# Performance work log

Measured on AMD Instinct MI355X. Metric: run time of the kernel, lower is better.

## Reference

```python
import jax, jax.numpy as jnp
import numpy as np

NEG_SLOPE = 0.2
EPS = 1e-16


def _gat_conv(x_src, x_dst, src, dst, W_src, W_dst, a_src, a_dst, b):
    """Single-head bipartite GAT-style conv (gather-score-softmax-scatter)."""
    num_dst = x_dst.shape[0]
    h_src = x_src @ W_src                      # [Ns, C]
    h_dst = x_dst @ W_dst                      # [Nd, C]
    s_src = h_src @ a_src                      # [Ns]
    s_dst = h_dst @ a_dst                      # [Nd]
    e = jax.nn.leaky_relu(s_src[src] + s_dst[dst], NEG_SLOPE)  # [E]
    # segment softmax over incoming edges of each dst node
    m = jax.ops.segment_max(e, dst, num_segments=num_dst)      # [Nd]
    w = jnp.exp(e - m[dst])
    denom = jax.ops.segment_sum(w, dst, num_segments=num_dst)  # [Nd]
    alpha = w / (denom[dst] + EPS)                             # [E]
    out = jax.ops.segment_sum(alpha[:, None] * h_src[src], dst, num_segments=num_dst)
    return out + b


def setup_inputs() -> dict:
    key = jax.random.key(0)
    ks = jax.random.split(key, 32)
    N_a, N_p, N_v = 100000, 150000, 10000
    F_in, C = 768, 64
    E_w, E_c, E_p = 300000, 1500000, 150000
    sc_in = 1.0 / np.sqrt(F_in)
    sc_c = 1.0 / np.sqrt(C)
    inp = {
        'x_author': jax.random.normal(ks[0], (N_a, F_in), jnp.float32),
        'x_paper': jax.random.normal(ks[1], (N_p, F_in), jnp.float32),
        'x_venue': jax.random.normal(ks[2], (N_v, F_in), jnp.float32),
        'writes_src': jax.random.randint(ks[3], (E_w,), 0, N_a, jnp.int32),
        'writes_dst': jax.random.randint(ks[4], (E_w,), 0, N_p, jnp.int32),
        'cites_src': jax.random.randint(ks[5], (E_c,), 0, N_p, jnp.int32),
        'cites_dst': jax.random.randint(ks[6], (E_c,), 0, N_p, jnp.int32),
        'pub_src': jax.random.randint(ks[7], (E_p,), 0, N_v, jnp.int32),
        'pub_dst': jax.random.randint(ks[8], (E_p,), 0, N_p, jnp.int32),
    }
    # per-edge-type learned params: W_src, W_dst [F_in, C], att vecs [C], bias [C]
    names = ['w', 'c', 'p']  # writes, cites, publishes
    for i, n in enumerate(names):
        base = 9 + 5 * i
        inp[f'W{n}_src'] = jax.random.normal(ks[base + 0], (F_in, C), jnp.float32) * sc_in
        inp[f'W{n}_dst'] = jax.random.normal(ks[base + 1], (F_in, C), jnp.float32) * sc_in
        inp[f'a{n}_src'] = jax.random.normal(ks[base + 2], (C,), jnp.float32) * sc_c
        inp[f'a{n}_dst'] = jax.random.normal(ks[base + 3], (C,), jnp.float32) * sc_c
        inp[f'b{n}'] = jnp.zeros((C,), jnp.float32)
    return inp


def reference(x_author, x_paper, x_venue,
              writes_src, writes_dst, cites_src, cites_dst, pub_src, pub_dst,
              Ww_src, Ww_dst, aw_src, aw_dst, bw,
              Wc_src, Wc_dst, ac_src, ac_dst, bc,
              Wp_src, Wp_dst, ap_src, ap_dst, bp):
    # HeteroConv with aggr='sum': all three edge types target 'paper'
    out_w = _gat_conv(x_author, x_paper, writes_src, writes_dst, Ww_src, Ww_dst, aw_src, aw_dst, bw)
    out_c = _gat_conv(x_paper, x_paper, cites_src, cites_dst, Wc_src, Wc_dst, ac_src, ac_dst, bc)
    out_p = _gat_conv(x_venue, x_paper, pub_src, pub_dst, Wp_src, Wp_dst, ap_src, ap_dst, bp)
    return out_w + out_c + out_p  # [N_paper, out_channels]
```

## Files before the change

### kernel.cpp

```cpp
#include <hip/hip_runtime.h>


#define F_IN 768
#define C_OUT 64
#define BN 80
#define TILE_M 64
#define BK 64
#define LDK 72

typedef __bf16 bf16x8 __attribute__((ext_vector_type(8)));
typedef float  f32x4  __attribute__((ext_vector_type(4)));

__global__ void prep_weights(
    const float* __restrict__ Ww_src, const float* __restrict__ aw_src,
    const float* __restrict__ Wc_src, const float* __restrict__ ac_src,
    const float* __restrict__ Wp_src, const float* __restrict__ ap_src,
    const float* __restrict__ Ww_dst, const float* __restrict__ aw_dst,
    const float* __restrict__ Wc_dst, const float* __restrict__ ac_dst,
    const float* __restrict__ Wp_dst, const float* __restrict__ ap_dst,
    __bf16* __restrict__ WTw, __bf16* __restrict__ WTc, __bf16* __restrict__ WTp)
{
    int type = blockIdx.x;
    const float* Ws = (type == 0) ? Ww_src : (type == 1) ? Wc_src : Wp_src;
    const float* as = (type == 0) ? aw_src : (type == 1) ? ac_src : ap_src;
    __bf16* WT = (type == 0) ? WTw : (type == 1) ? WTc : WTp;

    for (int r = threadIdx.x; r < F_IN; r += blockDim.x) {
        const float* wrow = Ws + (size_t)r * C_OUT;
        float u = 0.f;
        for (int c = 0; c < C_OUT; ++c) {
            float wv = wrow[c];
            WT[(size_t)c * F_IN + r] = (__bf16)wv;
            u += wv * as[c];
        }
        WT[(size_t)64 * F_IN + r] = (__bf16)u;
        for (int c = 65; c < BN; ++c) WT[(size_t)c * F_IN + r] = (__bf16)0.f;
        if (type == 1) {
            const float* r1 = Ww_dst + (size_t)r * C_OUT;
            const float* r2 = Wc_dst + (size_t)r * C_OUT;
            const float* r3 = Wp_dst + (size_t)r * C_OUT;
            float vw = 0.f, vc = 0.f, vp = 0.f;
            for (int c = 0; c < C_OUT; ++c) {
                vw += r1[c] * aw_dst[c];
                vc += r2[c] * ac_dst[c];
                vp += r3[c] * ap_dst[c];
            }
            WT[(size_t)65 * F_IN + r] = (__bf16)vw;
            WT[(size_t)66 * F_IN + r] = (__bf16)vc;
            WT[(size_t)67 * F_IN + r] = (__bf16)vp;
        }
    }
}

__global__ __launch_bounds__(256) void gemm_fused(
    const float* __restrict__ X, const __bf16* __restrict__ WT,
    float* __restrict__ H,
    float* __restrict__ s0, float* __restrict__ s1,
    float* __restrict__ s2, float* __restrict__ s3, int M)
{
    __shared__ __bf16 As[TILE_M][LDK];
    __shared__ __bf16 Bs[BN][LDK];

    const int tid  = threadIdx.x;
    const int lane = tid & 63;
    const int warp = tid >> 6;
    const int colq = lane & 15;
    const int quad = lane >> 4;
    const int rowBase = blockIdx.x * TILE_M;

    f32x4 acc[5];
#pragma unroll
    for (int t = 0; t < 5; ++t) acc[t] = (f32x4){0.f, 0.f, 0.f, 0.f};

    const int arow  = tid >> 2;
    const int akoff = (tid & 3) * 16;
    const int grow  = rowBase + arow;
    const bool rowOK = grow < M;
    const float* xrow = X + (size_t)grow * F_IN;

    for (int kc = 0; kc < F_IN; kc += BK) {
        f32x4 av[4];
        if (rowOK) {
            const f32x4* xp = (const f32x4*)(xrow + kc + akoff);
            av[0] = xp[0]; av[1] = xp[1]; av[2] = xp[2]; av[3] = xp[3];
        } else {
#pragma unroll
            for (int i = 0; i < 4; ++i) av[i] = (f32x4){0.f, 0.f, 0.f, 0.f};
        }
        bf16x8 cv[2];
#pragma unroll
        for (int i = 0; i < 4; ++i)
#pragma unroll
            for (int j = 0; j < 4; ++j)
                cv[i >> 1][(i & 1) * 4 + j] = (__bf16)av[i][j];
        *(bf16x8*)&As[arow][akoff]     = cv[0];
        *(bf16x8*)&As[arow][akoff + 8] = cv[1];

        for (int c = tid; c < (BN * BK / 8); c += 256) {
            int br = c >> 3, bo = (c & 7) * 8;
            *(bf16x8*)&Bs[br][bo] =
                *(const bf16x8*)&WT[(size_t)br * F_IN + kc + bo];
        }
        __syncthreads();

#pragma unroll
        for (int kk = 0; kk < BK; kk += 32) {
            bf16x8 a = *(const bf16x8*)&As[warp * 16 + colq][kk + quad * 8];
#pragma unroll
            for (int t = 0; t < 5; ++t) {
                bf16x8 b = *(const bf16x8*)&Bs[t * 16 + colq][kk + quad * 8];
                acc[t] = __builtin_amdgcn_mfma_f32_16x16x32_bf16(a, b, acc[t], 0, 0, 0);
            }
        }
        __syncthreads();
    }

    const int orow0 = rowBase + warp * 16 + quad * 4;
#pragma unroll
    for (int r = 0; r < 4; ++r) {
        int row = orow0 + r;
        if (row < M) {
#pragma unroll
            for (int t = 0; t < 4; ++t)
                H[(size_t)row * C_OUT + t * 16 + colq] = acc[t][r];
            if (colq < 4) {
                float* sp = (colq == 0) ? s0 : (colq == 1) ? s1 : (colq == 2) ? s2 : s3;
                if (sp) sp[row] = acc[4][r];
            }
        }
    }
}

__global__ void init_out(const float* __restrict__ bw, const float* __restrict__ bc,
                         const float* __restrict__ bp, float* __restrict__ out, int n)
{
    int i = blockIdx.x * blockDim.x + threadIdx.x;
    if (i < n) {
        int c = i & 63;
        out[i] = bw[c] + bc[c] + bp[c];
    }
}

__global__ void edge_score(const float* __restrict__ sS, const float* __restrict__ sD,
                           const int* __restrict__ src, const int* __restrict__ dst,
                           float* __restrict__ wbuf, float* __restrict__ denom, int E)
{
    int i = blockIdx.x * blockDim.x + threadIdx.x;
    int stride = gridDim.x * blockDim.x;
    for (; i < E; i += stride) {
        float e = sS[src[i]] + sD[dst[i]];
        e = (e >= 0.f) ? e : 0.2f * e;
        float w = __expf(e);
        wbuf[i] = w;
        atomicAdd(&denom[dst[i]], w);
    }
}

__global__ void edge_scatter(const float* __restrict__ H, const float* __restrict__ wbuf,
                             const float* __restrict__ denom, const int* __restrict__ src,
                             const int* __restrict__ dst, float* __restrict__ out, int E)
{
    const int lane = threadIdx.x & 63;
    int wid = (blockIdx.x * blockDim.x + threadIdx.x) >> 6;
    const int nw = (gridDim.x * blockDim.x) >> 6;
    for (int e = wid; e < E; e += nw) {
        int s = src[e], d = dst[e];
        float alpha = wbuf[e] / (denom[d] + 1e-16f);
        float v = H[(size_t)s * C_OUT + lane] * alpha;
        atomicAdd(&out[(size_t)d * C_OUT + lane], v);
    }
}

extern "C" void kernel_launch(void* const* d_in, const int* in_sizes, int n_in,
                              void* d_out, int out_size, void* d_ws, size_t ws_size,
                              hipStream_t stream)
{
    const float* x_a = (const float*)d_in[0];
    const float* x_p = (const float*)d_in[1];
    const float* x_v = (const float*)d_in[2];
    const int* w_src = (const int*)d_in[3];
    const int* w_dst = (const int*)d_in[4];
    const int* c_src = (const int*)d_in[5];
    const int* c_dst = (const int*)d_in[6];
    const int* p_src = (const int*)d_in[7];
    const int* p_dst = (const int*)d_in[8];
    const float* Ww_src = (const float*)d_in[9];
    const float* Ww_dst = (const float*)d_in[10];
    const float* aw_src = (const float*)d_in[11];
    const float* aw_dst = (const float*)d_in[12];
    const float* bw     = (const float*)d_in[13];
    const float* Wc_src = (const float*)d_in[14];
    const float* Wc_dst = (const float*)d_in[15];
    const float* ac_src = (const float*)d_in[16];
    const float* ac_dst = (const float*)d_in[17];
    const float* bc     = (const float*)d_in[18];
    const float* Wp_src = (const float*)d_in[19];
    const float* Wp_dst = (const float*)d_in[20];
    const float* ap_src = (const float*)d_in[21];
    const float* ap_dst = (const float*)d_in[22];
    const float* bp     = (const float*)d_in[23];
    float* out = (float*)d_out;

    const int Na = in_sizes[0] / F_IN;
    const int Np = in_sizes[1] / F_IN;
    const int Nv = in_sizes[2] / F_IN;
    const int Ew = in_sizes[3];
    const int Ec = in_sizes[5];
    const int Ep = in_sizes[7];

    char* ws = (char*)d_ws;
    size_t off = 0;
    auto alloc = [&](size_t bytes) -> void* {
        off = (off + 255) & ~(size_t)255;
        void* p = ws + off;
        off += bytes;
        return p;
    };
    __bf16* WTw = (__bf16*)alloc((size_t)BN * F_IN * 2);
    __bf16* WTc = (__bf16*)alloc((size_t)BN * F_IN * 2);
    __bf16* WTp = (__bf16*)alloc((size_t)BN * F_IN * 2);
    float* Ha = (float*)alloc((size_t)Na * C_OUT * 4);
    float* Hp = (float*)alloc((size_t)Np * C_OUT * 4);
    float* Hv = (float*)alloc((size_t)Nv * C_OUT * 4);
    float* s_w_src = (float*)alloc((size_t)Na * 4);
    float* s_c_src = (float*)alloc((size_t)Np * 4);
    float* s_p_src = (float*)alloc((size_t)Nv * 4);
    float* s_w_dst = (float*)alloc((size_t)Np * 4);
    float* s_c_dst = (float*)alloc((size_t)Np * 4);
    float* s_p_dst = (float*)alloc((size_t)Np * 4);
    float* den = (float*)alloc((size_t)3 * Np * 4);
    float* den_w = den, *den_c = den + Np, *den_p = den + 2 * Np;
    float* wb_w = (float*)alloc((size_t)Ew * 4);
    float* wb_c = (float*)alloc((size_t)Ec * 4);
    float* wb_p = (float*)alloc((size_t)Ep * 4);
    (void)ws_size; (void)n_in; (void)out_size;

    hipMemsetAsync(den, 0, (size_t)3 * Np * 4, stream);

    prep_weights<<<3, 256, 0, stream>>>(
        Ww_src, aw_src, Wc_src, ac_src, Wp_src, ap_src,
        Ww_dst, aw_dst, Wc_dst, ac_dst, Wp_dst, ap_dst,
        WTw, WTc, WTp);

    gemm_fused<<<(Na + TILE_M - 1) / TILE_M, 256, 0, stream>>>(
        x_a, WTw, Ha, s_w_src, nullptr, nullptr, nullptr, Na);
    gemm_fused<<<(Np + TILE_M - 1) / TILE_M, 256, 0, stream>>>(
        x_p, WTc, Hp, s_c_src, s_w_dst, s_c_dst, s_p_dst, Np);
    gemm_fused<<<(Nv + TILE_M - 1) / TILE_M, 256, 0, stream>>>(
        x_v, WTp, Hv, s_p_src, nullptr, nullptr, nullptr, Nv);

    init_out<<<(Np * C_OUT + 255) / 256, 256, 0, stream>>>(bw, bc, bp, out, Np * C_OUT);

    edge_score<<<1024, 256, 0, stream>>>(s_w_src, s_w_dst, w_src, w_dst, wb_w, den_w, Ew);
    edge_score<<<2048, 256, 0, stream>>>(s_c_src, s_c_dst, c_src, c_dst, wb_c, den_c, Ec);
    edge_score<<<1024, 256, 0, stream>>>(s_p_src, s_p_dst, p_src, p_dst, wb_p, den_p, Ep);

    edge_scatter<<<2048, 256, 0, stream>>>(Ha, wb_w, den_w, w_src, w_dst, out, Ew);
    edge_scatter<<<4096, 256, 0, stream>>>(Hp, wb_c, den_c, c_src, c_dst, out, Ec);
    edge_scatter<<<2048, 256, 0, stream>>>(Hv, wb_p, den_p, p_src, p_dst, out, Ep);
}
```

Before: 1.482 ms.

## Replace atomic edge scatter with CSR-by-destination gather and fused softmax

Builds a CSR index of all three edge types grouped by destination paper, using a histogram, a three-pass prefix scan and a counting-sort scatter. A single gather kernel then computes scores, exp weights, per-type denominators and weighted feature sums per destination in one wavefront, and adds the bias. This removes the per-edge float atomics on the 64-wide output rows, the denominator atomics and the edge weight buffers. In exchange it adds several small sort and scan kernels plus integer atomics on a cursor array, and it still uses no max subtraction, as before.

```diff
diff --git a/kernel.cpp b/kernel.cpp
--- a/kernel.cpp
+++ b/kernel.cpp
@@ -7,6 +7,7 @@
 #define TILE_M 64
 #define BK 64
 #define LDK 72
+#define EPS 1e-16f
 
 typedef __bf16 bf16x8 __attribute__((ext_vector_type(8)));
 typedef float  f32x4  __attribute__((ext_vector_type(4)));
@@ -131,43 +132,168 @@
     }
 }
 
-__global__ void init_out(const float* __restrict__ bw, const float* __restrict__ bc,
-                         const float* __restrict__ bp, float* __restrict__ out, int n)
+__global__ void hist3(const int* __restrict__ d1, int E1,
+                      const int* __restrict__ d2, int E2,
+                      const int* __restrict__ d3, int E3,
+                      int* __restrict__ cnt)
+{
+    int i0 = blockIdx.x * blockDim.x + threadIdx.x;
+    int stride = gridDim.x * blockDim.x;
+    for (int i = i0; i < E1; i += stride) atomicAdd(&cnt[d1[i]], 1);
+    for (int i = i0; i < E2; i += stride) atomicAdd(&cnt[d2[i]], 1);
+    for (int i = i0; i < E3; i += stride) atomicAdd(&cnt[d3[i]], 1);
+}
+
+__global__ void scan1(const int* __restrict__ cnt, int n,
+                      int* __restrict__ rowptr, int* __restrict__ bsums)
+{
+    __shared__ int sm[256];
+    const int t = threadIdx.x;
+    const int base = blockIdx.x * 1024 + t * 4;
+    int v[4];
+    int tot = 0;
+#pragma unroll
+    for (int k = 0; k < 4; ++k) {
+        v[k] = (base + k < n) ? cnt[base + k] : 0;
+        tot += v[k];
+    }
+    sm[t] = tot;
+    __syncthreads();
+    for (int off = 1; off < 256; off <<= 1) {
+        int add = (t >= off) ? sm[t - off] : 0;
+        __syncthreads();
+        sm[t] += add;
+        __syncthreads();
+    }
+    int run = sm[t] - tot;
+#pragma unroll
+    for (int k = 0; k < 4; ++k) {
+        if (base + k < n) rowptr[base + k] = run;
+        run += v[k];
+    }
+    if (t == 255) bsums[blockIdx.x] = sm[255];
+}
+
+__global__ void scan2(int* __restrict__ bsums, int nb)
+{
+    __shared__ int sm[256];
+    const int t = threadIdx.x;
+    int v = (t < nb) ? bsums[t] : 0;
+    sm[t] = v;
+    __syncthreads();
+    for (int off = 1; off < 256; off <<= 1) {
+        int add = (t >= off) ? sm[t - off] : 0;
+        __syncthreads();
+        sm[t] += add;
+        __syncthreads();
+    }
+    if (t < nb) bsums[t] = sm[t] - v;
+}
+
+__global__ void scan3(const int* __restrict__ bsums, int n, int Etot,
+                      int* __restrict__ rowptr, int* __restrict__ cursor)
 {
     int i = blockIdx.x * blockDim.x + threadIdx.x;
     if (i < n) {
-        int c = i & 63;
-        out[i] = bw[c] + bc[c] + bp[c];
-    }
-}
-
-__global__ void edge_score(const float* __restrict__ sS, const float* __restrict__ sD,
-                           const int* __restrict__ src, const int* __restrict__ dst,
-                           float* __restrict__ wbuf, float* __restrict__ denom, int E)
-{
-    int i = blockIdx.x * blockDim.x + threadIdx.x;
+        int r = rowptr[i] + bsums[i >> 10];
+        rowptr[i] = r;
+        cursor[i] = r;
+    }
+    if (i == 0) rowptr[n] = Etot;
+}
+
+__global__ void edge_sort3(const int* __restrict__ s1, const int* __restrict__ d1, int E1,
+                           const int* __restrict__ s2, const int* __restrict__ d2, int E2,
+                           const int* __restrict__ s3, const int* __restrict__ d3, int E3,
+                           int* __restrict__ cursor, unsigned* __restrict__ eidx)
+{
+    int i0 = blockIdx.x * blockDim.x + threadIdx.x;
     int stride = gridDim.x * blockDim.x;
-    for (; i < E; i += stride) {
-        float e = sS[src[i]] + sD[dst[i]];
-        e = (e >= 0.f) ? e : 0.2f * e;
-        float w = __expf(e);
-        wbuf[i] = w;
-        atomicAdd(&denom[dst[i]], w);
-    }
-}
-
-__global__ void edge_scatter(const float* __restrict__ H, const float* __restrict__ wbuf,
-                             const float* __restrict__ denom, const int* __restrict__ src,
-                             const int* __restrict__ dst, float* __restrict__ out, int E)
+    for (int i = i0; i < E1; i += stride) {
+        int p = atomicAdd(&cursor[d1[i]], 1);
+        eidx[p] = (0u << 24) | (unsigned)s1[i];
+    }
+    for (int i = i0; i < E2; i += stride) {
+        int p = atomicAdd(&cursor[d2[i]], 1);
+        eidx[p] = (1u << 24) | (unsigned)s2[i];
+    }
+    for (int i = i0; i < E3; i += stride) {
+        int p = atomicAdd(&cursor[d3[i]], 1);
+        eidx[p] = (2u << 24) | (unsigned)s3[i];
+    }
+}
+
+__global__ __launch_bounds__(256) void gat_gather(
+    const unsigned* __restrict__ eidx, const int* __restrict__ rowptr,
+    const float* __restrict__ Ha, const float* __restrict__ Hp, const float* __restrict__ Hv,
+    const float* __restrict__ ssw, const float* __restrict__ ssc, const float* __restrict__ ssp,
+    const float* __restrict__ sdw, const float* __restrict__ sdc, const float* __restrict__ sdp,
+    const float* __restrict__ bw, const float* __restrict__ bc, const float* __restrict__ bp,
+    float* __restrict__ out, int Nd)
 {
     const int lane = threadIdx.x & 63;
-    int wid = (blockIdx.x * blockDim.x + threadIdx.x) >> 6;
+    const int wid = (blockIdx.x * blockDim.x + threadIdx.x) >> 6;
     const int nw = (gridDim.x * blockDim.x) >> 6;
-    for (int e = wid; e < E; e += nw) {
-        int s = src[e], d = dst[e];
-        float alpha = wbuf[e] / (denom[d] + 1e-16f);
-        float v = H[(size_t)s * C_OUT + lane] * alpha;
-        atomicAdd(&out[(size_t)d * C_OUT + lane], v);
+    const float bsum = bw[lane] + bc[lane] + bp[lane];
+
+    for (int d = wid; d < Nd; d += nw) {
+        const int start = rowptr[d];
+        const int end   = rowptr[d + 1];
+        const float sd0 = sdw[d], sd1 = sdc[d], sd2 = sdp[d];
+        float a0 = 0.f, a1 = 0.f, a2 = 0.f;
+        float dn0 = 0.f, dn1 = 0.f, dn2 = 0.f;
+
+        for (int base = start; base < end; base += 64) {
+            int n = end - base;
+            if (n > 64) n = 64;
+            unsigned ew = 0u;
+            float w = 0.f;
+            if (lane < n) {
+                ew = eidx[base + lane];
+                int t = (int)(ew >> 24);
+                int s = (int)(ew & 0xFFFFFFu);
+                float ss = (t == 0) ? ssw[s] : (t == 1) ? ssc[s] : ssp[s];
+                float sd = (t == 0) ? sd0 : (t == 1) ? sd1 : sd2;
+                float e = ss + sd;
+                e = (e >= 0.f) ? e : 0.2f * e;
+                w = __expf(e);
+                if (t == 0) dn0 += w; else if (t == 1) dn1 += w; else dn2 += w;
+            }
+            int j = 0;
+            for (; j + 4 <= n; j += 4) {
+#pragma unroll
+                for (int u = 0; u < 4; ++u) {
+                    float wj = __shfl(w, j + u);
+                    unsigned ej = (unsigned)__shfl((int)ew, j + u);
+                    int tj = (int)(ej >> 24);
+                    int sj = (int)(ej & 0xFFFFFFu);
+                    const float* Hr = (tj == 0) ? Ha : (tj == 1) ? Hp : Hv;
+                    float hv = Hr[(size_t)sj * C_OUT + lane];
+                    if (tj == 0) a0 += wj * hv;
+                    else if (tj == 1) a1 += wj * hv;
+                    else a2 += wj * hv;
+                }
+            }
+            for (; j < n; ++j) {
+                float wj = __shfl(w, j);
+                unsigned ej = (unsigned)__shfl((int)ew, j);
+                int tj = (int)(ej >> 24);
+                int sj = (int)(ej & 0xFFFFFFu);
+                const float* Hr = (tj == 0) ? Ha : (tj == 1) ? Hp : Hv;
+                float hv = Hr[(size_t)sj * C_OUT + lane];
+                if (tj == 0) a0 += wj * hv;
+                else if (tj == 1) a1 += wj * hv;
+                else a2 += wj * hv;
+            }
+        }
+#pragma unroll
+        for (int off = 32; off > 0; off >>= 1) {
+            dn0 += __shfl_xor(dn0, off);
+            dn1 += __shfl_xor(dn1, off);
+            dn2 += __shfl_xor(dn2, off);
+        }
+        out[(size_t)d * C_OUT + lane] =
+            a0 / (dn0 + EPS) + a1 / (dn1 + EPS) + a2 / (dn2 + EPS) + bsum;
     }
 }
 
@@ -207,6 +333,7 @@
     const int Ew = in_sizes[3];
     const int Ec = in_sizes[5];
     const int Ep = in_sizes[7];
+    const int Etot = Ew + Ec + Ep;
 
     char* ws = (char*)d_ws;
     size_t off = 0;
@@ -228,14 +355,14 @@
     float* s_w_dst = (float*)alloc((size_t)Np * 4);
     float* s_c_dst = (float*)alloc((size_t)Np * 4);
     float* s_p_dst = (float*)alloc((size_t)Np * 4);
-    float* den = (float*)alloc((size_t)3 * Np * 4);
-    float* den_w = den, *den_c = den + Np, *den_p = den + 2 * Np;
-    float* wb_w = (float*)alloc((size_t)Ew * 4);
-    float* wb_c = (float*)alloc((size_t)Ec * 4);
-    float* wb_p = (float*)alloc((size_t)Ep * 4);
+    int* cnt    = (int*)alloc((size_t)Np * 4);
+    int* rowptr = (int*)alloc((size_t)(Np + 1) * 4);
+    int* cursor = (int*)alloc((size_t)Np * 4);
+    int* bsums  = (int*)alloc(1024);
+    unsigned* eidx = (unsigned*)alloc((size_t)Etot * 4);
     (void)ws_size; (void)n_in; (void)out_size;
 
-    hipMemsetAsync(den, 0, (size_t)3 * Np * 4, stream);
+    hipMemsetAsync(cnt, 0, (size_t)Np * 4, stream);
 
     prep_weights<<<3, 256, 0, stream>>>(
         Ww_src, aw_src, Wc_src, ac_src, Wp_src, ap_src,
@@ -249,13 +376,16 @@
     gemm_fused<<<(Nv + TILE_M - 1) / TILE_M, 256, 0, stream>>>(
         x_v, WTp, Hv, s_p_src, nullptr, nullptr, nullptr, Nv);
 
-    init_out<<<(Np * C_OUT + 255) / 256, 256, 0, stream>>>(bw, bc, bp, out, Np * C_OUT);
-
-    edge_score<<<1024, 256, 0, stream>>>(s_w_src, s_w_dst, w_src, w_dst, wb_w, den_w, Ew);
-    edge_score<<<2048, 256, 0, stream>>>(s_c_src, s_c_dst, c_src, c_dst, wb_c, den_c, Ec);
-    edge_score<<<1024, 256, 0, stream>>>(s_p_src, s_p_dst, p_src, p_dst, wb_p, den_p, Ep);
-
-    edge_scatter<<<2048, 256, 0, stream>>>(Ha, wb_w, den_w, w_src, w_dst, out, Ew);
-    edge_scatter<<<4096, 256, 0, stream>>>(Hp, wb_c, den_c, c_src, c_dst, out, Ec);
-    edge_scatter<<<2048, 256, 0, stream>>>(Hv, wb_p, den_p, p_src, p_dst, out, Ep);
-}
+    hist3<<<1024, 256, 0, stream>>>(w_dst, Ew, c_dst, Ec, p_dst, Ep, cnt);
+    const int NB = (Np + 1023) / 1024;
+    scan1<<<NB, 256, 0, stream>>>(cnt, Np, rowptr, bsums);
+    scan2<<<1, 256, 0, stream>>>(bsums, NB);
+    scan3<<<(Np + 255) / 256, 256, 0, stream>>>(bsums, Np, Etot, rowptr, cursor);
+    edge_sort3<<<1024, 256, 0, stream>>>(
+        w_src, w_dst, Ew, c_src, c_dst, Ec, p_src, p_dst, Ep, cursor, eidx);
+
+    gat_gather<<<2048, 256, 0, stream>>>(
+        eidx, rowptr, Ha, Hp, Hv,
+        s_w_src, s_c_src, s_p_src, s_w_dst, s_c_dst, s_p_dst,
+        bw, bc, bp, out, Np);
+}
```

Result: faster. 1.349 ms (-8.9%).
